# Performance work log

Measured on AMD Instinct MI355X. Metric: run time of the kernel, lower is better.

The kernel has to match this reference:

```python
import jax, jax.numpy as jnp
import numpy as np

N = 50000        # nodes
E = 600000       # edges (before self-loops)
VOCAB = 100000
EMB = 128
HID = 128
G = 64           # graphs in batch
NEG_SLOPE = 0.2


def setup_inputs() -> dict:
    key = jax.random.key(0)
    ks = jax.random.split(key, 16)
    x_idx = jax.random.randint(ks[0], (N,), 0, VOCAB)
    edge_index = jax.random.randint(ks[1], (2, E), 0, N)
    edge_attr = jax.random.uniform(ks[2], (E,), dtype=jnp.float32)
    batch = jnp.sort(jax.random.randint(ks[3], (N,), 0, G))
    # embedding table; padding_idx=0 row zeroed as in nn.Embedding(padding_idx=0)
    emb_table = (jax.random.normal(ks[4], (VOCAB, EMB), dtype=jnp.float32) * 0.05).at[0].set(0.0)
    glorot = lambda k, shp: jax.random.normal(k, shp, dtype=jnp.float32) * np.float32(np.sqrt(2.0 / sum(shp)))
    W1 = glorot(ks[5], (HID, EMB))
    att_src1 = glorot(ks[6], (HID,)) * 0.0 + jax.random.normal(ks[6], (HID,), dtype=jnp.float32) * np.float32(np.sqrt(2.0 / (HID + 1)))
    att_dst1 = jax.random.normal(ks[7], (HID,), dtype=jnp.float32) * np.float32(np.sqrt(2.0 / (HID + 1)))
    W2 = glorot(ks[8], (HID, HID))
    att_src2 = jax.random.normal(ks[9], (HID,), dtype=jnp.float32) * np.float32(np.sqrt(2.0 / (HID + 1)))
    att_dst2 = jax.random.normal(ks[10], (HID,), dtype=jnp.float32) * np.float32(np.sqrt(2.0 / (HID + 1)))
    W3 = glorot(ks[11], (HID // 2, HID))
    b3 = jnp.zeros((HID // 2,), jnp.float32)
    W4 = glorot(ks[12], (2, HID // 2))
    b4 = jnp.zeros((2,), jnp.float32)
    return {"x_idx": x_idx, "edge_index": edge_index, "edge_attr": edge_attr, "batch": batch,
            "emb_table": emb_table, "W1": W1, "att_src1": att_src1, "att_dst1": att_dst1,
            "W2": W2, "att_src2": att_src2, "att_dst2": att_dst2,
            "W3": W3, "b3": b3, "W4": W4, "b4": b4}


def _segment_softmax(logits, seg, n):
    m = jax.ops.segment_max(logits, seg, num_segments=n)
    e = jnp.exp(logits - m[seg])
    s = jax.ops.segment_sum(e, seg, num_segments=n)
    return e / (s[seg] + 1e-16)


def _edge_attr_gat_conv(x, src, dst, ea, W, a_src, a_dst, n):
    H = x @ W.T                                   # [n, out]
    # per-edge score: (H_i . a_dst) + (H_j . a_src); compute per-node then gather
    alpha = (H @ a_dst)[dst] + (H @ a_src)[src]   # [e]
    alpha = jnp.where(alpha >= 0, alpha, NEG_SLOPE * alpha)
    alpha = alpha * ea                            # multiplicative edge attr
    alpha = _segment_softmax(alpha, dst, n)       # softmax over in-neighborhoods
    return jax.ops.segment_sum(H[src] * alpha[:, None], dst, num_segments=n)


def reference(x_idx, edge_index, edge_attr, batch, emb_table,
              W1, att_src1, att_dst1, W2, att_src2, att_dst2, W3, b3, W4, b4):
    n = x_idx.shape[0]
    loops = jnp.arange(n)
    # add_self_loops (done inside each conv in torch; same edges both layers)
    src = jnp.concatenate([edge_index[0], loops])
    dst = jnp.concatenate([edge_index[1], loops])  # edge_index_i (aggregation index)
    ea = jnp.concatenate([edge_attr, jnp.ones((n,), edge_attr.dtype)])
    x = emb_table[x_idx]
    x = jax.nn.relu(_edge_attr_gat_conv(x, src, dst, ea, W1, att_src1, att_dst1, n))
    x = jax.nn.relu(_edge_attr_gat_conv(x, src, dst, ea, W2, att_src2, att_dst2, n))
    # global_mean_pool
    sums = jax.ops.segment_sum(x, batch, num_segments=G)
    counts = jax.ops.segment_sum(jnp.ones((n,), x.dtype), batch, num_segments=G)
    g = sums / jnp.maximum(counts, 1.0)[:, None]
    # MLP head (dropout = identity at eval)
    h = jax.nn.relu(g @ W3.T + b3)
    return h @ W4.T + b4
```

## Files before the change

kernel.cpp:

```cpp
#include <hip/hip_runtime.h>
#include <cstdint>
#include <cstddef>


#define CSR_CHUNK 8192
#define NXCD 8

__device__ __forceinline__ float wave_sum(float v) {
#pragma unroll
  for (int m = 32; m >= 1; m >>= 1) v += __shfl_xor(v, m, 64);
  return v;
}


__global__ void init_kernel(int* __restrict__ deg, float* __restrict__ gsum,
                            const int* __restrict__ batch,
                            int* __restrict__ gstart, int* __restrict__ gend,
                            int N, int G) {
  int i = blockIdx.x * blockDim.x + threadIdx.x;
  if (i < N) {
    deg[i] = 1;
    int b = batch[i];
    if (i == 0 || batch[i - 1] != b) gstart[b] = i;
    if (i == N - 1 || batch[i + 1] != b) gend[b] = i + 1;
  }
  if (i < G * 128) gsum[i] = 0.f;
}

__global__ void count_deg_part_kernel(const int* __restrict__ edge_index,
                                      int* __restrict__ deg, int E, int RN) {
  int r = blockIdx.x & (NXCD - 1);
  int s = blockIdx.x >> 3;
  int lo = r * RN, hi = lo + RN;
  int e1 = min(E, (s + 1) * CSR_CHUNK);
  for (int e = s * CSR_CHUNK + threadIdx.x; e < e1; e += blockDim.x) {
    int d = edge_index[E + e];
    if (d >= lo && d < hi) atomicAdd(&deg[d], 1);
  }
}

__global__ void scan1_kernel(const int* __restrict__ deg, int* __restrict__ bsum, int N) {
  __shared__ int ws[4];
  int tid = threadIdx.x;
  int i = blockIdx.x * 256 + tid;
  int v = (i < N) ? deg[i] : 0;
#pragma unroll
  for (int m = 32; m >= 1; m >>= 1) v += __shfl_xor(v, m, 64);
  if ((tid & 63) == 0) ws[tid >> 6] = v;
  __syncthreads();
  if (tid == 0) bsum[blockIdx.x] = ws[0] + ws[1] + ws[2] + ws[3];
}

__device__ __forceinline__ int block_excl_scan_256(int v, int tid, int* wsum) {
  int lane = tid & 63, wid = tid >> 6;
  int incl = v;
#pragma unroll
  for (int off = 1; off < 64; off <<= 1) {
    int t = __shfl_up(incl, off, 64);
    if (lane >= off) incl += t;
  }
  if (lane == 63) wsum[wid] = incl;
  __syncthreads();
  int woff = 0;
#pragma unroll
  for (int w = 0; w < 4; ++w)
    if (w < wid) woff += wsum[w];
  return woff + incl - v;
}

__global__ void scan2_kernel(const int* __restrict__ bsum, int* __restrict__ boff,
                             int* __restrict__ row_ptr, int nb, int N) {
  __shared__ int wsum[4];
  int tid = threadIdx.x;
  int v = (tid < nb) ? bsum[tid] : 0;
  int excl = block_excl_scan_256(v, tid, wsum);
  if (tid < nb) boff[tid] = excl;
  if (tid == 255) row_ptr[N] = excl + v;
}

__global__ void scan3_fill_kernel(const int* __restrict__ deg, const int* __restrict__ boff,
                                  int* __restrict__ row_ptr, int2* __restrict__ pk,
                                  int* __restrict__ cur, int N) {
  __shared__ int wsum[4];
  int tid = threadIdx.x;
  int i = blockIdx.x * 256 + tid;
  int v = (i < N) ? deg[i] : 0;
  int excl = block_excl_scan_256(v, tid, wsum);
  if (i < N) {
    int p = boff[blockIdx.x] + excl;
    row_ptr[i] = p;
    pk[p] = make_int2(i, __float_as_int(1.0f));
    cur[i] = p + 1;
  }
}

__global__ void fillB_part_kernel(const int* __restrict__ edge_index,
                                  const float* __restrict__ ea,
                                  int* __restrict__ cur, int2* __restrict__ pk,
                                  int E, int RN) {
  int r = blockIdx.x & (NXCD - 1);
  int s = blockIdx.x >> 3;
  int lo = r * RN, hi = lo + RN;
  int e1 = min(E, (s + 1) * CSR_CHUNK);
  for (int e = s * CSR_CHUNK + threadIdx.x; e < e1; e += blockDim.x) {
    int d = edge_index[E + e];
    if (d >= lo && d < hi) {
      int s0 = edge_index[e];
      float a0 = ea[e];
      int p = atomicAdd(&cur[d], 1);
      pk[p] = make_int2(s0, __float_as_int(a0));
    }
  }
}


__global__ __launch_bounds__(256) void gemm_att_kernel(
    const float* __restrict__ Xin, const int* __restrict__ gidx,
    const float* __restrict__ W,
    const float* __restrict__ a_src, const float* __restrict__ a_dst,
    float* __restrict__ H, float* __restrict__ sv, float* __restrict__ dv, int N) {
  __shared__ float XsT[32][128];
  __shared__ float Wt[32][128];
  __shared__ float av[2][128];

  int tid = threadIdx.x;
  int tx = tid & 15, ty = tid >> 4;
  int rb = blockIdx.x * 128;

  if (tid < 128) { av[0][tid] = a_src[tid]; av[1][tid] = a_dst[tid]; }

  int r0 = tid & 127;
  int q0 = tid >> 7;
  int gr0 = rb + r0; if (gr0 >= N) gr0 = N - 1;
  const float* rp0 = gidx ? (Xin + (size_t)gidx[gr0] * 128) : (Xin + (size_t)gr0 * 128);
  const float* wp0 = W + (size_t)r0 * 128;

  float acc[8][8];
#pragma unroll
  for (int r = 0; r < 8; ++r)
#pragma unroll
    for (int j = 0; j < 8; ++j) acc[r][j] = 0.f;

#pragma unroll
  for (int ks = 0; ks < 4; ++ks) {
    const int k0 = ks * 32;
    __syncthreads();
#pragma unroll
    for (int it = 0; it < 4; ++it) {
      int q = q0 + it * 2;
      float4 v = *(const float4*)(rp0 + k0 + q * 4);
      XsT[q * 4 + 0][r0] = v.x; XsT[q * 4 + 1][r0] = v.y;
      XsT[q * 4 + 2][r0] = v.z; XsT[q * 4 + 3][r0] = v.w;
      float4 u = *(const float4*)(wp0 + k0 + q * 4);
      Wt[q * 4 + 0][r0] = u.x; Wt[q * 4 + 1][r0] = u.y;
      Wt[q * 4 + 2][r0] = u.z; Wt[q * 4 + 3][r0] = u.w;
    }
    __syncthreads();
#pragma unroll 2
    for (int k = 0; k < 32; ++k) {
      float4 xa0 = *(const float4*)&XsT[k][ty * 8];
      float4 xa1 = *(const float4*)&XsT[k][ty * 8 + 4];
      float4 wb0 = *(const float4*)&Wt[k][tx * 8];
      float4 wb1 = *(const float4*)&Wt[k][tx * 8 + 4];
      float xr[8] = {xa0.x, xa0.y, xa0.z, xa0.w, xa1.x, xa1.y, xa1.z, xa1.w};
      float wc[8] = {wb0.x, wb0.y, wb0.z, wb0.w, wb1.x, wb1.y, wb1.z, wb1.w};
#pragma unroll
      for (int r = 0; r < 8; ++r)
#pragma unroll
        for (int j = 0; j < 8; ++j) acc[r][j] = fmaf(xr[r], wc[j], acc[r][j]);
    }
  }

#pragma unroll
  for (int r = 0; r < 8; ++r) {
    int gr = rb + ty * 8 + r;
    float ps = 0.f, pd = 0.f;
#pragma unroll
    for (int j = 0; j < 8; ++j) {
      ps = fmaf(acc[r][j], av[0][tx * 8 + j], ps);
      pd = fmaf(acc[r][j], av[1][tx * 8 + j], pd);
    }
#pragma unroll
    for (int m = 1; m < 16; m <<= 1) {
      ps += __shfl_xor(ps, m, 64);
      pd += __shfl_xor(pd, m, 64);
    }
    if (gr < N) {
      float4 lo = make_float4(acc[r][0], acc[r][1], acc[r][2], acc[r][3]);
      float4 hi = make_float4(acc[r][4], acc[r][5], acc[r][6], acc[r][7]);
      *(float4*)(H + (size_t)gr * 128 + tx * 8) = lo;
      *(float4*)(H + (size_t)gr * 128 + tx * 8 + 4) = hi;
      if (tx == 0) { sv[gr] = ps; dv[gr] = pd; }
    }
  }
}


__global__ __launch_bounds__(256) void agg_kernel(
    const float* __restrict__ H, const float* __restrict__ sv, const float* __restrict__ dv,
    const int* __restrict__ row_ptr, const int2* __restrict__ pk,
    float* __restrict__ Xout, int N) {
  int tid = threadIdx.x;
  int hw = tid >> 5;
  int cl = tid & 31;
  int node = blockIdx.x * 8 + hw;
  if (node >= N) return;
  int p0 = row_ptr[node], p1 = row_ptr[node + 1];
  int deg = p1 - p0;
  float di = dv[node];

  float4 acc = make_float4(0.f, 0.f, 0.f, 0.f);
  float S = 0.f;

  if (deg <= 32) {
    float f = -3.4e38f; int sE = 0;
    if (cl < deg) {
      int2 pe = pk[p0 + cl];
      sE = pe.x;
      float t = di + sv[sE];
      t = (t >= 0.f) ? t : 0.2f * t;
      f = t * __int_as_float(pe.y);
    }
    float m = f;
#pragma unroll
    for (int s = 16; s >= 1; s >>= 1) m = fmaxf(m, __shfl_xor(m, s, 32));
    float w = (cl < deg) ? expf(f - m) : 0.f;
    float Ss = w;
#pragma unroll
    for (int s = 16; s >= 1; s >>= 1) Ss += __shfl_xor(Ss, s, 32);
    S = Ss;
    for (int t0 = 0; t0 < deg; t0 += 4) {
      float4 v[4]; float wv[4];
#pragma unroll
      for (int u = 0; u < 4; ++u) {
        int idx = t0 + u;
        float wj = __shfl(w, idx, 32);
        int sj = __shfl(sE, idx, 32);
        bool valid = idx < deg;
        wv[u] = valid ? wj : 0.f;
        const float4* hr = (const float4*)(H + (size_t)(valid ? sj : 0) * 128);
        v[u] = hr[cl];
      }
#pragma unroll
      for (int u = 0; u < 4; ++u) {
        acc.x = fmaf(wv[u], v[u].x, acc.x);
        acc.y = fmaf(wv[u], v[u].y, acc.y);
        acc.z = fmaf(wv[u], v[u].z, acc.z);
        acc.w = fmaf(wv[u], v[u].w, acc.w);
      }
    }
  } else {
    float m = -3.4e38f;
    for (int p = p0; p < p1; p += 32) {
      int e = p + cl;
      float f = -3.4e38f;
      if (e < p1) {
        int2 pe = pk[e];
        float t = di + sv[pe.x];
        t = (t >= 0.f) ? t : 0.2f * t;
        f = t * __int_as_float(pe.y);
      }
#pragma unroll
      for (int s = 16; s >= 1; s >>= 1) f = fmaxf(f, __shfl_xor(f, s, 32));
      m = fmaxf(m, f);
    }
    for (int p = p0; p < p1; p += 32) {
      int cnt = min(32, p1 - p);
      float w = 0.f; int sE = 0;
      if (cl < cnt) {
        int2 pe = pk[p + cl];
        sE = pe.x;
        float t = di + sv[sE];
        t = (t >= 0.f) ? t : 0.2f * t;
        w = expf(t * __int_as_float(pe.y) - m);
      }
      float Ss = w;
#pragma unroll
      for (int s = 16; s >= 1; s >>= 1) Ss += __shfl_xor(Ss, s, 32);
      S += Ss;
      for (int t0 = 0; t0 < cnt; t0 += 4) {
        float4 v[4]; float wv[4];
#pragma unroll
        for (int u = 0; u < 4; ++u) {
          int idx = t0 + u;
          float wj = __shfl(w, idx, 32);
          int sj = __shfl(sE, idx, 32);
          bool valid = idx < cnt;
          wv[u] = valid ? wj : 0.f;
          const float4* hr = (const float4*)(H + (size_t)(valid ? sj : 0) * 128);
          v[u] = hr[cl];
        }
#pragma unroll
        for (int u = 0; u < 4; ++u) {
          acc.x = fmaf(wv[u], v[u].x, acc.x);
          acc.y = fmaf(wv[u], v[u].y, acc.y);
          acc.z = fmaf(wv[u], v[u].z, acc.z);
          acc.w = fmaf(wv[u], v[u].w, acc.w);
        }
      }
    }
  }

  float sc = 1.0f / (S + 1e-16f);
  float4 o;
  o.x = fmaxf(acc.x * sc, 0.f);
  o.y = fmaxf(acc.y * sc, 0.f);
  o.z = fmaxf(acc.z * sc, 0.f);
  o.w = fmaxf(acc.w * sc, 0.f);
  *(float4*)(Xout + (size_t)node * 128 + cl * 4) = o;
}


__global__ void pool_kernel(const float* __restrict__ X, const int* __restrict__ batch,
                            float* __restrict__ gsum, int N) {
  int col = threadIdx.x & 127;
  int half = threadIdx.x >> 7;
  int base = blockIdx.x * 128;
  int cur = -1; float acc = 0.f;
  for (int j = half; j < 128; j += 2) {
    int n = base + j;
    if (n >= N) break;
    int g = batch[n];
    if (g != cur) {
      if (cur >= 0) atomicAdd(&gsum[cur * 128 + col], acc);
      cur = g; acc = 0.f;
    }
    acc += X[(size_t)n * 128 + col];
  }
  if (cur >= 0) atomicAdd(&gsum[cur * 128 + col], acc);
}

__global__ __launch_bounds__(256) void head_kernel(
    const float* __restrict__ gsum,
    const int* __restrict__ gstart, const int* __restrict__ gend,
    const float* __restrict__ W3, const float* __restrict__ b3,
    const float* __restrict__ W4, const float* __restrict__ b4,
    float* __restrict__ out, int G) {
  __shared__ float gv[128];
  __shared__ float h[64];
  int gid = blockIdx.x;
  int tid = threadIdx.x;
  float cnt = (float)(gend[gid] - gstart[gid]);
  if (cnt < 1.f) cnt = 1.f;
  if (tid < 128) gv[tid] = gsum[(size_t)gid * 128 + tid] / cnt;
  __syncthreads();
  {
    int c = tid >> 2, part = tid & 3;
    const float4* w = (const float4*)(W3 + (size_t)c * 128 + part * 32);
    const float4* gg = (const float4*)(gv + part * 32);
    float acc = 0.f;
#pragma unroll
    for (int k = 0; k < 8; ++k) {
      float4 a = gg[k], b = w[k];
      acc = fmaf(a.x, b.x, acc); acc = fmaf(a.y, b.y, acc);
      acc = fmaf(a.z, b.z, acc); acc = fmaf(a.w, b.w, acc);
    }
    acc += __shfl_xor(acc, 1, 64);
    acc += __shfl_xor(acc, 2, 64);
    if (part == 0) { float v = acc + b3[c]; h[c] = (v > 0.f) ? v : 0.f; }
  }
  __syncthreads();
  if (tid < 128) {
    int o = tid >> 6, k = tid & 63;
    float p = h[k] * W4[o * 64 + k];
    p = wave_sum(p);
    if (k == 0) out[gid * 2 + o] = p + b4[o];
  }
}


extern "C" void kernel_launch(void* const* d_in, const int* in_sizes, int n_in,
                              void* d_out, int out_size, void* d_ws, size_t ws_size,
                              hipStream_t stream) {
  const int* x_idx = (const int*)d_in[0];
  const int* edge_index = (const int*)d_in[1];
  const float* edge_attr = (const float*)d_in[2];
  const int* batch = (const int*)d_in[3];
  const float* emb = (const float*)d_in[4];
  const float* W1 = (const float*)d_in[5];
  const float* as1 = (const float*)d_in[6];
  const float* ad1 = (const float*)d_in[7];
  const float* W2 = (const float*)d_in[8];
  const float* as2 = (const float*)d_in[9];
  const float* ad2 = (const float*)d_in[10];
  const float* W3 = (const float*)d_in[11];
  const float* b3 = (const float*)d_in[12];
  const float* W4 = (const float*)d_in[13];
  const float* b4 = (const float*)d_in[14];

  const int N = in_sizes[0];
  const int E = in_sizes[2];
  const int G = out_size / 2;
  const int ET = E + N;

  uint8_t* wp = (uint8_t*)d_ws;
  auto take = [&](size_t bytes) -> void* {
    void* p = (void*)wp;
    wp += (bytes + 255) & ~(size_t)255;
    return p;
  };
  float* H    = (float*)take((size_t)N * 128 * 4);
  float* X    = (float*)take((size_t)N * 128 * 4);
  float* sv   = (float*)take((size_t)N * 4);
  float* dv   = (float*)take((size_t)N * 4);
  int*   deg  = (int*)take((size_t)N * 4);
  int*   rowp = (int*)take((size_t)(N + 1) * 4);
  int*   cur  = (int*)take((size_t)N * 4);
  int*   bsum = (int*)take(256 * 4);
  int*   boff = (int*)take(256 * 4);
  int2*  pk   = (int2*)take((size_t)ET * 8);
  float* gsum = (float*)take((size_t)G * 128 * 4);
  int*   gstart = (int*)take((size_t)G * 4);
  int*   gend   = (int*)take((size_t)G * 4);
  (void)ws_size; (void)n_in;

  const int nb = (N + 255) / 256;
  const int RN = (N + NXCD - 1) / NXCD;
  const int ns = (E + CSR_CHUNK - 1) / CSR_CHUNK;
  const int pb = ns * NXCD;

  init_kernel<<<nb, 256, 0, stream>>>(deg, gsum, batch, gstart, gend, N, G);
  count_deg_part_kernel<<<pb, 256, 0, stream>>>(edge_index, deg, E, RN);
  scan1_kernel<<<nb, 256, 0, stream>>>(deg, bsum, N);
  scan2_kernel<<<1, 256, 0, stream>>>(bsum, boff, rowp, nb, N);
  scan3_fill_kernel<<<nb, 256, 0, stream>>>(deg, boff, rowp, pk, cur, N);
  fillB_part_kernel<<<pb, 256, 0, stream>>>(edge_index, edge_attr, cur, pk, E, RN);

  const int gb = (N + 127) / 128;
  const int ab = (N + 7) / 8;
  gemm_att_kernel<<<gb, 256, 0, stream>>>(emb, x_idx, W1, as1, ad1, H, sv, dv, N);
  agg_kernel<<<ab, 256, 0, stream>>>(H, sv, dv, rowp, pk, X, N);
  gemm_att_kernel<<<gb, 256, 0, stream>>>(X, nullptr, W2, as2, ad2, H, sv, dv, N);
  agg_kernel<<<ab, 256, 0, stream>>>(H, sv, dv, rowp, pk, X, N);
  pool_kernel<<<(N + 127) / 128, 256, 0, stream>>>(X, batch, gsum, N);
  head_kernel<<<G, 256, 0, stream>>>(gsum, gstart, gend, W3, b3, W4, b4, (float*)d_out, G);
}
```

Baseline: 274.6 us.

## Merge CSR build into one cooperative kernel and fuse pooling into head

Replaces the six CSR-construction launches (init, degree count, three scan stages, fill) with one cooperative kernel of 512 blocks that separates the phases with grid-wide syncs. The separate pooling kernel and its atomics are removed: the head kernel now has 512 threads and sums each graph's contiguous node range directly, relying on the sorted batch vector. The goal is to cut launch gaps and atomic traffic. In exchange, 512 blocks must fit co-resident for the cooperative launch, and the pooling reads become serial per graph, with only 64 blocks scanning all of X.

```diff
diff --git a/kernel.cpp b/kernel.cpp
--- a/kernel.cpp
+++ b/kernel.cpp
@@ -1,7 +1,10 @@
 #include <hip/hip_runtime.h>
+#include <hip/hip_cooperative_groups.h>
 #include <cstdint>
 #include <cstddef>
 
+namespace cg = cooperative_groups;
+
 
 #define CSR_CHUNK 8192
 #define NXCD 8
@@ -13,102 +16,112 @@
 }
 
 
-__global__ void init_kernel(int* __restrict__ deg, float* __restrict__ gsum,
-                            const int* __restrict__ batch,
-                            int* __restrict__ gstart, int* __restrict__ gend,
-                            int N, int G) {
-  int i = blockIdx.x * blockDim.x + threadIdx.x;
-  if (i < N) {
-    deg[i] = 1;
+__global__ __launch_bounds__(256, 2) void csr_coop_kernel(
+    const int* __restrict__ edge_index, const float* __restrict__ ea,
+    const int* __restrict__ batch,
+    int* __restrict__ deg, int* __restrict__ bsum, int* __restrict__ boff,
+    int* __restrict__ rowp, int2* __restrict__ pk, int* __restrict__ cur,
+    int* __restrict__ gstart, int* __restrict__ gend,
+    int N, int E, int G, int RN, int ns, int nb) {
+  cg::grid_group gg = cg::this_grid();
+  __shared__ int ws[4];
+  int tid = threadIdx.x;
+  int gtid = blockIdx.x * 256 + tid;
+  int gsz = gridDim.x * 256;
+
+  for (int i = gtid; i < N; i += gsz) deg[i] = 1;
+  if (gtid < G) { gstart[gtid] = 0; gend[gtid] = 0; }
+  gg.sync();
+
+  for (int i = gtid; i < N; i += gsz) {
     int b = batch[i];
     if (i == 0 || batch[i - 1] != b) gstart[b] = i;
     if (i == N - 1 || batch[i + 1] != b) gend[b] = i + 1;
   }
-  if (i < G * 128) gsum[i] = 0.f;
-}
-
-__global__ void count_deg_part_kernel(const int* __restrict__ edge_index,
-                                      int* __restrict__ deg, int E, int RN) {
-  int r = blockIdx.x & (NXCD - 1);
-  int s = blockIdx.x >> 3;
-  int lo = r * RN, hi = lo + RN;
-  int e1 = min(E, (s + 1) * CSR_CHUNK);
-  for (int e = s * CSR_CHUNK + threadIdx.x; e < e1; e += blockDim.x) {
-    int d = edge_index[E + e];
-    if (d >= lo && d < hi) atomicAdd(&deg[d], 1);
-  }
-}
-
-__global__ void scan1_kernel(const int* __restrict__ deg, int* __restrict__ bsum, int N) {
-  __shared__ int ws[4];
-  int tid = threadIdx.x;
-  int i = blockIdx.x * 256 + tid;
-  int v = (i < N) ? deg[i] : 0;
-#pragma unroll
-  for (int m = 32; m >= 1; m >>= 1) v += __shfl_xor(v, m, 64);
-  if ((tid & 63) == 0) ws[tid >> 6] = v;
-  __syncthreads();
-  if (tid == 0) bsum[blockIdx.x] = ws[0] + ws[1] + ws[2] + ws[3];
-}
-
-__device__ __forceinline__ int block_excl_scan_256(int v, int tid, int* wsum) {
-  int lane = tid & 63, wid = tid >> 6;
-  int incl = v;
-#pragma unroll
-  for (int off = 1; off < 64; off <<= 1) {
-    int t = __shfl_up(incl, off, 64);
-    if (lane >= off) incl += t;
-  }
-  if (lane == 63) wsum[wid] = incl;
-  __syncthreads();
-  int woff = 0;
-#pragma unroll
-  for (int w = 0; w < 4; ++w)
-    if (w < wid) woff += wsum[w];
-  return woff + incl - v;
-}
-
-__global__ void scan2_kernel(const int* __restrict__ bsum, int* __restrict__ boff,
-                             int* __restrict__ row_ptr, int nb, int N) {
-  __shared__ int wsum[4];
-  int tid = threadIdx.x;
-  int v = (tid < nb) ? bsum[tid] : 0;
-  int excl = block_excl_scan_256(v, tid, wsum);
-  if (tid < nb) boff[tid] = excl;
-  if (tid == 255) row_ptr[N] = excl + v;
-}
-
-__global__ void scan3_fill_kernel(const int* __restrict__ deg, const int* __restrict__ boff,
-                                  int* __restrict__ row_ptr, int2* __restrict__ pk,
-                                  int* __restrict__ cur, int N) {
-  __shared__ int wsum[4];
-  int tid = threadIdx.x;
-  int i = blockIdx.x * 256 + tid;
-  int v = (i < N) ? deg[i] : 0;
-  int excl = block_excl_scan_256(v, tid, wsum);
-  if (i < N) {
-    int p = boff[blockIdx.x] + excl;
-    row_ptr[i] = p;
-    pk[p] = make_int2(i, __float_as_int(1.0f));
-    cur[i] = p + 1;
-  }
-}
-
-__global__ void fillB_part_kernel(const int* __restrict__ edge_index,
-                                  const float* __restrict__ ea,
-                                  int* __restrict__ cur, int2* __restrict__ pk,
-                                  int E, int RN) {
-  int r = blockIdx.x & (NXCD - 1);
-  int s = blockIdx.x >> 3;
-  int lo = r * RN, hi = lo + RN;
-  int e1 = min(E, (s + 1) * CSR_CHUNK);
-  for (int e = s * CSR_CHUNK + threadIdx.x; e < e1; e += blockDim.x) {
-    int d = edge_index[E + e];
-    if (d >= lo && d < hi) {
-      int s0 = edge_index[e];
-      float a0 = ea[e];
-      int p = atomicAdd(&cur[d], 1);
-      pk[p] = make_int2(s0, __float_as_int(a0));
+  for (int vb = blockIdx.x; vb < ns * NXCD; vb += gridDim.x) {
+    int r = vb & (NXCD - 1), s = vb >> 3;
+    int lo = r * RN, hi = lo + RN;
+    int e1 = min(E, (s + 1) * CSR_CHUNK);
+    for (int e = s * CSR_CHUNK + tid; e < e1; e += 256) {
+      int d = edge_index[E + e];
+      if (d >= lo && d < hi) atomicAdd(&deg[d], 1);
+    }
+  }
+  gg.sync();
+
+  for (int vb = blockIdx.x; vb < nb; vb += gridDim.x) {
+    int i = vb * 256 + tid;
+    int v = (i < N) ? deg[i] : 0;
+#pragma unroll
+    for (int m = 32; m >= 1; m >>= 1) v += __shfl_xor(v, m, 64);
+    if ((tid & 63) == 0) ws[tid >> 6] = v;
+    __syncthreads();
+    if (tid == 0) bsum[vb] = ws[0] + ws[1] + ws[2] + ws[3];
+    __syncthreads();
+  }
+  gg.sync();
+
+  if (blockIdx.x == 0) {
+    int v = (tid < nb) ? bsum[tid] : 0;
+    int lane = tid & 63, wid = tid >> 6;
+    int incl = v;
+#pragma unroll
+    for (int off = 1; off < 64; off <<= 1) {
+      int t = __shfl_up(incl, off, 64);
+      if (lane >= off) incl += t;
+    }
+    if (lane == 63) ws[wid] = incl;
+    __syncthreads();
+    int woff = 0;
+#pragma unroll
+    for (int w = 0; w < 4; ++w)
+      if (w < wid) woff += ws[w];
+    int excl = woff + incl - v;
+    if (tid < nb) boff[tid] = excl;
+    if (tid == 255) rowp[N] = excl + v;
+    __syncthreads();
+  }
+  gg.sync();
+
+  for (int vb = blockIdx.x; vb < nb; vb += gridDim.x) {
+    int i = vb * 256 + tid;
+    int v = (i < N) ? deg[i] : 0;
+    int lane = tid & 63, wid = tid >> 6;
+    int incl = v;
+#pragma unroll
+    for (int off = 1; off < 64; off <<= 1) {
+      int t = __shfl_up(incl, off, 64);
+      if (lane >= off) incl += t;
+    }
+    if (lane == 63) ws[wid] = incl;
+    __syncthreads();
+    int woff = 0;
+#pragma unroll
+    for (int w = 0; w < 4; ++w)
+      if (w < wid) woff += ws[w];
+    int excl = woff + incl - v;
+    if (i < N) {
+      int p = boff[vb] + excl;
+      rowp[i] = p;
+      pk[p] = make_int2(i, __float_as_int(1.0f));
+      cur[i] = p + 1;
+    }
+    __syncthreads();
+  }
+  gg.sync();
+
+  for (int vb = blockIdx.x; vb < ns * NXCD; vb += gridDim.x) {
+    int r = vb & (NXCD - 1), s = vb >> 3;
+    int lo = r * RN, hi = lo + RN;
+    int e1 = min(E, (s + 1) * CSR_CHUNK);
+    for (int e = s * CSR_CHUNK + tid; e < e1; e += 256) {
+      int d = edge_index[E + e];
+      if (d >= lo && d < hi) {
+        int s0 = edge_index[e];
+        float a0 = ea[e];
+        int p = atomicAdd(&cur[d], 1);
+        pk[p] = make_int2(s0, __float_as_int(a0));
+      }
     }
   }
 }
@@ -311,53 +324,43 @@
 }
 
 
-__global__ void pool_kernel(const float* __restrict__ X, const int* __restrict__ batch,
-                            float* __restrict__ gsum, int N) {
-  int col = threadIdx.x & 127;
-  int half = threadIdx.x >> 7;
-  int base = blockIdx.x * 128;
-  int cur = -1; float acc = 0.f;
-  for (int j = half; j < 128; j += 2) {
-    int n = base + j;
-    if (n >= N) break;
-    int g = batch[n];
-    if (g != cur) {
-      if (cur >= 0) atomicAdd(&gsum[cur * 128 + col], acc);
-      cur = g; acc = 0.f;
-    }
-    acc += X[(size_t)n * 128 + col];
-  }
-  if (cur >= 0) atomicAdd(&gsum[cur * 128 + col], acc);
-}
-
-__global__ __launch_bounds__(256) void head_kernel(
-    const float* __restrict__ gsum,
+__global__ __launch_bounds__(512) void head_kernel(
+    const float* __restrict__ X,
     const int* __restrict__ gstart, const int* __restrict__ gend,
     const float* __restrict__ W3, const float* __restrict__ b3,
     const float* __restrict__ W4, const float* __restrict__ b4,
     float* __restrict__ out, int G) {
+  __shared__ float sums[4][128];
   __shared__ float gv[128];
   __shared__ float h[64];
   int gid = blockIdx.x;
   int tid = threadIdx.x;
-  float cnt = (float)(gend[gid] - gstart[gid]);
+  int s0 = gstart[gid], e0 = gend[gid];
+  float cnt = (float)(e0 - s0);
   if (cnt < 1.f) cnt = 1.f;
-  if (tid < 128) gv[tid] = gsum[(size_t)gid * 128 + tid] / cnt;
+
+  int col = tid & 127, rg = tid >> 7;
+  float acc = 0.f;
+  for (int n = s0 + rg; n < e0; n += 4) acc += X[(size_t)n * 128 + col];
+  sums[rg][col] = acc;
   __syncthreads();
-  {
+  if (tid < 128) gv[tid] = (sums[0][tid] + sums[1][tid] + sums[2][tid] + sums[3][tid]) / cnt;
+  __syncthreads();
+
+  if (tid < 256) {
     int c = tid >> 2, part = tid & 3;
     const float4* w = (const float4*)(W3 + (size_t)c * 128 + part * 32);
     const float4* gg = (const float4*)(gv + part * 32);
-    float acc = 0.f;
+    float a = 0.f;
 #pragma unroll
     for (int k = 0; k < 8; ++k) {
-      float4 a = gg[k], b = w[k];
-      acc = fmaf(a.x, b.x, acc); acc = fmaf(a.y, b.y, acc);
-      acc = fmaf(a.z, b.z, acc); acc = fmaf(a.w, b.w, acc);
-    }
-    acc += __shfl_xor(acc, 1, 64);
-    acc += __shfl_xor(acc, 2, 64);
-    if (part == 0) { float v = acc + b3[c]; h[c] = (v > 0.f) ? v : 0.f; }
+      float4 x = gg[k], b = w[k];
+      a = fmaf(x.x, b.x, a); a = fmaf(x.y, b.y, a);
+      a = fmaf(x.z, b.z, a); a = fmaf(x.w, b.w, a);
+    }
+    a += __shfl_xor(a, 1, 64);
+    a += __shfl_xor(a, 2, 64);
+    if (part == 0) { float v = a + b3[c]; h[c] = (v > 0.f) ? v : 0.f; }
   }
   __syncthreads();
   if (tid < 128) {
@@ -409,7 +412,6 @@
   int*   bsum = (int*)take(256 * 4);
   int*   boff = (int*)take(256 * 4);
   int2*  pk   = (int2*)take((size_t)ET * 8);
-  float* gsum = (float*)take((size_t)G * 128 * 4);
   int*   gstart = (int*)take((size_t)G * 4);
   int*   gend   = (int*)take((size_t)G * 4);
   (void)ws_size; (void)n_in;
@@ -417,14 +419,19 @@
   const int nb = (N + 255) / 256;
   const int RN = (N + NXCD - 1) / NXCD;
   const int ns = (E + CSR_CHUNK - 1) / CSR_CHUNK;
-  const int pb = ns * NXCD;
-
-  init_kernel<<<nb, 256, 0, stream>>>(deg, gsum, batch, gstart, gend, N, G);
-  count_deg_part_kernel<<<pb, 256, 0, stream>>>(edge_index, deg, E, RN);
-  scan1_kernel<<<nb, 256, 0, stream>>>(deg, bsum, N);
-  scan2_kernel<<<1, 256, 0, stream>>>(bsum, boff, rowp, nb, N);
-  scan3_fill_kernel<<<nb, 256, 0, stream>>>(deg, boff, rowp, pk, cur, N);
-  fillB_part_kernel<<<pb, 256, 0, stream>>>(edge_index, edge_attr, cur, pk, E, RN);
+
+  {
+    int Nv = N, Ev = E, Gv = G, RNv = RN, nsv = ns, nbv = nb;
+    void* args[] = {
+      (void*)&edge_index, (void*)&edge_attr, (void*)&batch,
+      (void*)&deg, (void*)&bsum, (void*)&boff,
+      (void*)&rowp, (void*)&pk, (void*)&cur,
+      (void*)&gstart, (void*)&gend,
+      (void*)&Nv, (void*)&Ev, (void*)&Gv, (void*)&RNv, (void*)&nsv, (void*)&nbv
+    };
+    hipLaunchCooperativeKernel((const void*)csr_coop_kernel,
+                               dim3(512), dim3(256), args, 0, stream);
+  }
 
   const int gb = (N + 127) / 128;
   const int ab = (N + 7) / 8;
@@ -432,6 +439,5 @@
   agg_kernel<<<ab, 256, 0, stream>>>(H, sv, dv, rowp, pk, X, N);
   gemm_att_kernel<<<gb, 256, 0, stream>>>(X, nullptr, W2, as2, ad2, H, sv, dv, N);
   agg_kernel<<<ab, 256, 0, stream>>>(H, sv, dv, rowp, pk, X, N);
-  pool_kernel<<<(N + 127) / 128, 256, 0, stream>>>(X, batch, gsum, N);
-  head_kernel<<<G, 256, 0, stream>>>(gsum, gstart, gend, W3, b3, W4, b4, (float*)d_out, G);
-}
+  head_kernel<<<G, 512, 0, stream>>>(X, gstart, gend, W3, b3, W4, b4, (float*)d_out, G);
+}
```

After: 561.2 us. +104.4%, slower.

## Fuse mean pooling into head kernel with binary search for graph bounds

Applied to the files above, without the earlier changes.

Removes the separate atomic pool kernel and the gstart/gend/gsum setup in init. Each head block now binary-searches the sorted batch array for its graph range and sums that graph's rows directly with 512 threads. This saves a launch and the global atomics, but only 64 blocks read all of X (about 25 MB), which may underuse the GPU compared with the many-block pool kernel.

```diff
diff --git a/kernel.cpp b/kernel.cpp
--- a/kernel.cpp
+++ b/kernel.cpp
@@ -13,18 +13,9 @@
 }
 
 
-__global__ void init_kernel(int* __restrict__ deg, float* __restrict__ gsum,
-                            const int* __restrict__ batch,
-                            int* __restrict__ gstart, int* __restrict__ gend,
-                            int N, int G) {
+__global__ void init_kernel(int* __restrict__ deg, int N) {
   int i = blockIdx.x * blockDim.x + threadIdx.x;
-  if (i < N) {
-    deg[i] = 1;
-    int b = batch[i];
-    if (i == 0 || batch[i - 1] != b) gstart[b] = i;
-    if (i == N - 1 || batch[i + 1] != b) gend[b] = i + 1;
-  }
-  if (i < G * 128) gsum[i] = 0.f;
+  if (i < N) deg[i] = 1;
 }
 
 __global__ void count_deg_part_kernel(const int* __restrict__ edge_index,
@@ -311,53 +302,54 @@
 }
 
 
-__global__ void pool_kernel(const float* __restrict__ X, const int* __restrict__ batch,
-                            float* __restrict__ gsum, int N) {
-  int col = threadIdx.x & 127;
-  int half = threadIdx.x >> 7;
-  int base = blockIdx.x * 128;
-  int cur = -1; float acc = 0.f;
-  for (int j = half; j < 128; j += 2) {
-    int n = base + j;
-    if (n >= N) break;
-    int g = batch[n];
-    if (g != cur) {
-      if (cur >= 0) atomicAdd(&gsum[cur * 128 + col], acc);
-      cur = g; acc = 0.f;
-    }
-    acc += X[(size_t)n * 128 + col];
-  }
-  if (cur >= 0) atomicAdd(&gsum[cur * 128 + col], acc);
-}
-
-__global__ __launch_bounds__(256) void head_kernel(
-    const float* __restrict__ gsum,
-    const int* __restrict__ gstart, const int* __restrict__ gend,
+__global__ __launch_bounds__(512) void head_kernel(
+    const float* __restrict__ X, const int* __restrict__ batch, int N,
     const float* __restrict__ W3, const float* __restrict__ b3,
     const float* __restrict__ W4, const float* __restrict__ b4,
     float* __restrict__ out, int G) {
+  __shared__ int bounds[2];
+  __shared__ float sums[4][128];
   __shared__ float gv[128];
   __shared__ float h[64];
   int gid = blockIdx.x;
   int tid = threadIdx.x;
-  float cnt = (float)(gend[gid] - gstart[gid]);
+
+  if (tid < 2) {
+    int target = gid + tid;
+    int lo = 0, hi = N;
+    while (lo < hi) {
+      int mid = (lo + hi) >> 1;
+      if (batch[mid] < target) lo = mid + 1; else hi = mid;
+    }
+    bounds[tid] = lo;
+  }
+  __syncthreads();
+  int s0 = bounds[0], e0 = bounds[1];
+  float cnt = (float)(e0 - s0);
   if (cnt < 1.f) cnt = 1.f;
-  if (tid < 128) gv[tid] = gsum[(size_t)gid * 128 + tid] / cnt;
-  __syncthreads();
-  {
+
+  int col = tid & 127, rg = tid >> 7;
+  float acc = 0.f;
+  for (int n = s0 + rg; n < e0; n += 4) acc += X[(size_t)n * 128 + col];
+  sums[rg][col] = acc;
+  __syncthreads();
+  if (tid < 128) gv[tid] = (sums[0][tid] + sums[1][tid] + sums[2][tid] + sums[3][tid]) / cnt;
+  __syncthreads();
+
+  if (tid < 256) {
     int c = tid >> 2, part = tid & 3;
     const float4* w = (const float4*)(W3 + (size_t)c * 128 + part * 32);
     const float4* gg = (const float4*)(gv + part * 32);
-    float acc = 0.f;
+    float a = 0.f;
 #pragma unroll
     for (int k = 0; k < 8; ++k) {
-      float4 a = gg[k], b = w[k];
-      acc = fmaf(a.x, b.x, acc); acc = fmaf(a.y, b.y, acc);
-      acc = fmaf(a.z, b.z, acc); acc = fmaf(a.w, b.w, acc);
-    }
-    acc += __shfl_xor(acc, 1, 64);
-    acc += __shfl_xor(acc, 2, 64);
-    if (part == 0) { float v = acc + b3[c]; h[c] = (v > 0.f) ? v : 0.f; }
+      float4 x = gg[k], b = w[k];
+      a = fmaf(x.x, b.x, a); a = fmaf(x.y, b.y, a);
+      a = fmaf(x.z, b.z, a); a = fmaf(x.w, b.w, a);
+    }
+    a += __shfl_xor(a, 1, 64);
+    a += __shfl_xor(a, 2, 64);
+    if (part == 0) { float v = a + b3[c]; h[c] = (v > 0.f) ? v : 0.f; }
   }
   __syncthreads();
   if (tid < 128) {
@@ -409,9 +401,6 @@
   int*   bsum = (int*)take(256 * 4);
   int*   boff = (int*)take(256 * 4);
   int2*  pk   = (int2*)take((size_t)ET * 8);
-  float* gsum = (float*)take((size_t)G * 128 * 4);
-  int*   gstart = (int*)take((size_t)G * 4);
-  int*   gend   = (int*)take((size_t)G * 4);
   (void)ws_size; (void)n_in;
 
   const int nb = (N + 255) / 256;
@@ -419,7 +408,7 @@
   const int ns = (E + CSR_CHUNK - 1) / CSR_CHUNK;
   const int pb = ns * NXCD;
 
-  init_kernel<<<nb, 256, 0, stream>>>(deg, gsum, batch, gstart, gend, N, G);
+  init_kernel<<<nb, 256, 0, stream>>>(deg, N);
   count_deg_part_kernel<<<pb, 256, 0, stream>>>(edge_index, deg, E, RN);
   scan1_kernel<<<nb, 256, 0, stream>>>(deg, bsum, N);
   scan2_kernel<<<1, 256, 0, stream>>>(bsum, boff, rowp, nb, N);
@@ -432,6 +421,5 @@
   agg_kernel<<<ab, 256, 0, stream>>>(H, sv, dv, rowp, pk, X, N);
   gemm_att_kernel<<<gb, 256, 0, stream>>>(X, nullptr, W2, as2, ad2, H, sv, dv, N);
   agg_kernel<<<ab, 256, 0, stream>>>(H, sv, dv, rowp, pk, X, N);
-  pool_kernel<<<(N + 127) / 128, 256, 0, stream>>>(X, batch, gsum, N);
-  head_kernel<<<G, 256, 0, stream>>>(gsum, gstart, gend, W3, b3, W4, b4, (float*)d_out, G);
-}
+  head_kernel<<<G, 512, 0, stream>>>(X, batch, N, W3, b3, W4, b4, (float*)d_out, G);
+}
```

New measurement: 290.0 us. 5.6% more time.
